# Kernel optimization log

Measured on AMD Instinct MI355X. Metric: run time of the kernel, lower is better.

Reference implementation:

```python
import jax, jax.numpy as jnp
import numpy as np

NUM_EXPERTS = 8
CAPACITY_C = 1.0
ROUTER_TEMP = 1.0
EPS = 1e-10


def reference(x, router_w, router_b, w_gate, b_gate, w_up, b_up, w_down, b_down):
    # x: [B, S, H]
    B, S, H = x.shape
    n_tok = B * S
    k = int(n_tok * CAPACITY_C) // NUM_EXPERTS  # expert capacity (1024 here)

    xf = x.reshape(n_tok, H)  # (b s) h

    # Linear router (dropout p=0 -> identity), computed in float32 as in .float()
    clean_h = xf @ router_w + router_b  # [n_tok, E]

    # Gumbel noise (deterministic key stands in for torch.rand_like)
    u = jax.random.uniform(jax.random.key(42), clean_h.shape, dtype=clean_h.dtype)
    gumbel = -jnp.log(-jnp.log(u + EPS) + EPS)
    h = (clean_h + gumbel) / ROUTER_TEMP

    Sm = jax.nn.softmax(h, axis=-1)  # softmax over experts

    # top-k over the TOKEN dim (dim=0) per expert -> expert-choice routing
    Gt, idxt = jax.lax.top_k(Sm.T, k)  # [E, k]
    G = Gt.T            # [k, E] routing weights
    idx = idxt.T        # [k, E] chosen token indices

    # Gather routed tokens (replaces the one-hot einsum gather exactly:
    # top-k indices are distinct per expert, so one-hot matmul == take)
    toks = jnp.take(xf, idx, axis=0)  # [k, E, H]

    # Shared SwiGLU FFN (group_size=1 -> one expert instance reused E times)
    gate = jax.nn.silu(toks @ w_gate + b_gate)  # [k, E, dff]
    up = toks @ w_up + b_up                      # [k, E, dff]
    e_out = (gate * up) @ w_down + b_down        # [k, E, H]

    # Weight by G and scatter-add back to token positions, summed over experts
    weighted = G[..., None] * e_out              # [k, E, H]
    y = jnp.zeros_like(xf).at[idx.reshape(-1)].add(weighted.reshape(-1, H))
    return y.reshape(B, S, H)


def setup_inputs() -> dict:
    key = jax.random.key(0)
    ks = jax.random.split(key, 6)
    B, S, H, E = 4, 2048, 2048, NUM_EXPERTS
    dff = int(H * 4 * 2 / 3)  # 5461
    sH = 1.0 / np.sqrt(H)
    sF = 1.0 / np.sqrt(dff)
    return {
        "x": jax.random.normal(ks[0], (B, S, H), dtype=jnp.float32),
        "router_w": jax.random.normal(ks[1], (H, E), dtype=jnp.float32) * sH,
        "router_b": jnp.zeros((E,), dtype=jnp.float32),
        "w_gate": jax.random.normal(ks[2], (H, dff), dtype=jnp.float32) * sH,
        "b_gate": jnp.zeros((dff,), dtype=jnp.float32),
        "w_up": jax.random.normal(ks[3], (H, dff), dtype=jnp.float32) * sH,
        "b_up": jnp.zeros((dff,), dtype=jnp.float32),
        "w_down": jax.random.normal(ks[4], (dff, H), dtype=jnp.float32) * sF,
        "b_down": jnp.zeros((H,), dtype=jnp.float32),
    }
```

## Files before the change

### kernel.cpp

```cpp
#include <hip/hip_runtime.h>
#include <cstdint>
#include <cstddef>

#define N_TOK  8192
#define HDIM   2048
#define NEXP   8
#define KCAP   1024
#define DFF    5461
#define DFF_PB 5504
#define DFF_PA 5472

typedef unsigned short u16;
typedef short bf16x8 __attribute__((ext_vector_type(8)));
typedef float f32x4  __attribute__((ext_vector_type(4)));

__device__ __forceinline__ u16 f2bf(float f) {
  uint32_t u = __float_as_uint(f);
  uint32_t r = (u + 0x7FFFu + ((u >> 16) & 1u)) >> 16;
  return (u16)r;
}

__device__ __forceinline__ uint32_t rotl32(uint32_t v, int d) {
  return (v << d) | (v >> (32 - d));
}

__device__ uint32_t threefry_bits(uint32_t idx) {
  const uint32_t ks0 = 0u, ks1 = 42u, ks2 = 0u ^ 42u ^ 0x1BD11BDAu;
  uint32_t x0 = 0u + ks0;
  uint32_t x1 = idx + ks1;
#define TFR(d) { x0 += x1; x1 = rotl32(x1, d); x1 ^= x0; }
  TFR(13) TFR(15) TFR(26) TFR(6)
  x0 += ks1; x1 += ks2 + 1u;
  TFR(17) TFR(29) TFR(16) TFR(24)
  x0 += ks2; x1 += ks0 + 2u;
  TFR(13) TFR(15) TFR(26) TFR(6)
  x0 += ks0; x1 += ks1 + 3u;
  TFR(17) TFR(29) TFR(16) TFR(24)
  x0 += ks1; x1 += ks2 + 4u;
  TFR(13) TFR(15) TFR(26) TFR(6)
  x0 += ks2; x1 += ks0 + 5u;
#undef TFR
  return x0 ^ x1;
}

__global__ __launch_bounds__(256) void router_kernel(const float* __restrict__ x,
    const float* __restrict__ rw, const float* __restrict__ rb,
    float* __restrict__ SmT)
{
  const int lane = threadIdx.x & 63;
  const int wid  = threadIdx.x >> 6;
  const int t = blockIdx.x * 4 + wid;
  const float* xr = x + (size_t)t * HDIM;
  float acc[8] = {0.f,0.f,0.f,0.f,0.f,0.f,0.f,0.f};
#pragma unroll
  for (int it = 0; it < HDIM / 64; ++it) {
    int h = lane + it * 64;
    float xv = xr[h];
    const float4* wp = (const float4*)(rw + h * 8);
    float4 w0 = wp[0], w1 = wp[1];
    acc[0] = fmaf(xv, w0.x, acc[0]);
    acc[1] = fmaf(xv, w0.y, acc[1]);
    acc[2] = fmaf(xv, w0.z, acc[2]);
    acc[3] = fmaf(xv, w0.w, acc[3]);
    acc[4] = fmaf(xv, w1.x, acc[4]);
    acc[5] = fmaf(xv, w1.y, acc[5]);
    acc[6] = fmaf(xv, w1.z, acc[6]);
    acc[7] = fmaf(xv, w1.w, acc[7]);
  }
#pragma unroll
  for (int m = 32; m >= 1; m >>= 1) {
#pragma unroll
    for (int e = 0; e < 8; ++e) acc[e] += __shfl_xor(acc[e], m, 64);
  }
  if (lane == 0) {
    float h[8];
#pragma unroll
    for (int e = 0; e < 8; ++e) {
      uint32_t bits = threefry_bits((uint32_t)(t * 8 + e));
      float u = __uint_as_float((bits >> 9) | 0x3f800000u) - 1.0f;
      u = fmaxf(u, 0.0f);
      float g = -logf(-logf(u + 1e-10f) + 1e-10f);
      h[e] = acc[e] + rb[e] + g;
    }
    float mx = h[0];
#pragma unroll
    for (int e = 1; e < 8; ++e) mx = fmaxf(mx, h[e]);
    float ex[8]; float s = 0.f;
#pragma unroll
    for (int e = 0; e < 8; ++e) { ex[e] = expf(h[e] - mx); s += ex[e]; }
#pragma unroll
    for (int e = 0; e < 8; ++e) SmT[e * N_TOK + t] = ex[e] / s;
  }
}

__global__ __launch_bounds__(1024) void select_topk(const float* __restrict__ SmT,
    uint32_t* __restrict__ selTok, float* __restrict__ selW)
{
  const int e = blockIdx.x;
  const int tid = threadIdx.x;
  const float* v = SmT + (size_t)e * N_TOK;
  __shared__ uint32_t hist[256];
  __shared__ uint32_t sh_byte, sh_kk, sh_cnt, sh_eqc;
  uint32_t bitsv[8];
#pragma unroll
  for (int i = 0; i < 8; ++i) bitsv[i] = __float_as_uint(v[tid + i * 1024]);
  uint32_t prefix = 0;
  uint32_t kk = KCAP;
  for (int s = 3; s >= 0; --s) {
    if (tid < 256) hist[tid] = 0;
    __syncthreads();
    uint32_t himask = (s == 3) ? 0u : (0xFFFFFFFFu << ((s + 1) * 8));
#pragma unroll
    for (int i = 0; i < 8; ++i) {
      uint32_t b = bitsv[i];
      if ((b & himask) == prefix) atomicAdd(&hist[(b >> (s * 8)) & 255u], 1u);
    }
    __syncthreads();
    if (tid == 0) {
      uint32_t cum = 0; uint32_t bsel = 0, kn = kk;
      for (int b = 255; b >= 0; --b) {
        uint32_t c = hist[b];
        if (cum + c >= kk) { bsel = (uint32_t)b; kn = kk - cum; break; }
        cum += c;
      }
      sh_byte = bsel; sh_kk = kn;
    }
    __syncthreads();
    prefix |= sh_byte << (s * 8);
    kk = sh_kk;
  }
  const uint32_t T = prefix;
  const uint32_t need = kk;
  if (tid == 0) { sh_cnt = 0; sh_eqc = 0; }
  __syncthreads();
#pragma unroll
  for (int i = 0; i < 8; ++i) {
    uint32_t b = bitsv[i];
    if (b > T) {
      uint32_t p = atomicAdd(&sh_cnt, 1u);
      selTok[e * KCAP + p] = (uint32_t)(tid + i * 1024);
      selW[e * KCAP + p] = __uint_as_float(b);
    } else if (b == T) {
      atomicAdd(&sh_eqc, 1u);
    }
  }
  __syncthreads();
  if (sh_eqc == need) {
#pragma unroll
    for (int i = 0; i < 8; ++i) {
      if (bitsv[i] == T) {
        uint32_t p = atomicAdd(&sh_cnt, 1u);
        selTok[e * KCAP + p] = (uint32_t)(tid + i * 1024);
        selW[e * KCAP + p] = __uint_as_float(T);
      }
    }
  } else if (tid == 0) {
    uint32_t p = sh_cnt, rem = need;
    for (int t = 0; t < N_TOK && rem > 0u; ++t) {
      if (__float_as_uint(v[t]) == T) {
        selTok[e * KCAP + p] = (uint32_t)t;
        selW[e * KCAP + p] = __uint_as_float(T);
        ++p; --rem;
      }
    }
  }
}

__global__ __launch_bounds__(256) void gather_kernel(const float* __restrict__ x,
    const uint32_t* __restrict__ selTok, u16* __restrict__ Xsel)
{
  const int slot = blockIdx.x;
  const int tid = threadIdx.x;
  const uint32_t tok = selTok[slot];
  const float4* src = (const float4*)(x + (size_t)tok * HDIM);
  float4 a = src[tid * 2], b = src[tid * 2 + 1];
  union { u16 h[8]; uint4 vv; } pk;
  pk.h[0] = f2bf(a.x); pk.h[1] = f2bf(a.y); pk.h[2] = f2bf(a.z); pk.h[3] = f2bf(a.w);
  pk.h[4] = f2bf(b.x); pk.h[5] = f2bf(b.y); pk.h[6] = f2bf(b.z); pk.h[7] = f2bf(b.w);
  ((uint4*)(Xsel + (size_t)slot * HDIM))[tid] = pk.vv;
}

__global__ __launch_bounds__(256) void pad_act_kernel(u16* __restrict__ act) {
  int idx = blockIdx.x * 256 + threadIdx.x;
  int row = idx / 11, col = idx % 11;
  act[(size_t)row * DFF_PA + (DFF + col)] = 0;
}

__global__ __launch_bounds__(256) void transpose_convert(const float* __restrict__ in,
    int rows_in, int cols_in, u16* __restrict__ out, int out_cols)
{
  __shared__ float tile[32][33];
  const int bi = blockIdx.y;
  const int bj = blockIdx.x;
  const int tx = threadIdx.x, ty = threadIdx.y;
#pragma unroll
  for (int t = 0; t < 4; ++t) {
    int r = bi * 32 + ty + t * 8, c = bj * 32 + tx;
    float vv = (r < rows_in && c < cols_in) ? in[(size_t)r * cols_in + c] : 0.0f;
    tile[ty + t * 8][tx] = vv;
  }
  __syncthreads();
#pragma unroll
  for (int t = 0; t < 4; ++t) {
    int oj = bj * 32 + ty + t * 8;
    int oi = bi * 32 + tx;
    out[(size_t)oj * out_cols + oi] = f2bf(tile[tx][ty + t * 8]);
  }
}

#if defined(__has_builtin)
#  if __has_builtin(__builtin_amdgcn_global_load_lds)
#    define HAVE_GLD 1
#  endif
#endif
#ifdef HAVE_GLD
#define GLD16(gp, lp) __builtin_amdgcn_global_load_lds( \
    (const __attribute__((address_space(1))) void*)(gp), \
    (__attribute__((address_space(3))) void*)(lp), 16, 0, 0)
#endif

__global__ __launch_bounds__(256, 2) void gemm1_kernel(
    const u16* __restrict__ Xsel,
    const u16* __restrict__ WgT,
    const u16* __restrict__ WuT,
    const float* __restrict__ bg, const float* __restrict__ bu,
    u16* __restrict__ act)
{
  const int id = blockIdx.x;
  const int sc = id >> 9;
  const int rem = id & 511;
  const int bm = rem & 63;
  const int bn = sc * 8 + (rem >> 6);
  if (bn >= 86) return;

  __shared__ u16 As [128 * 32];
  __shared__ u16 Bgs[ 64 * 32];
  __shared__ u16 Bus[ 64 * 32];
  const int tid = threadIdx.x;
  const int lane = tid & 63, wid = tid >> 6;
  const int wr = wid >> 1, wc = wid & 1;
  const int c0 = tid, c1 = tid + 256;
  const int r0 = c0 >> 2, ko0 = ((c0 & 3) ^ (r0 & 3)) * 8;
  const int r1 = c1 >> 2, ko1 = ((c1 & 3) ^ (r1 & 3)) * 8;
  const int rbq = tid >> 2, kob = ((tid & 3) ^ (rbq & 3)) * 8;

  const u16* a_g0  = Xsel + (size_t)(bm * 128 + r0) * HDIM + ko0;
  const u16* a_g1  = Xsel + (size_t)(bm * 128 + r1) * HDIM + ko1;
  const u16* bg_g  = WgT  + (size_t)(bn * 64 + rbq) * HDIM + kob;
  const u16* bu_g  = WuT  + (size_t)(bn * 64 + rbq) * HDIM + kob;
  u16* a_l0 = As  + c0 * 8; u16* a_l1 = As + c1 * 8;
  u16* g_l  = Bgs + tid * 8;
  u16* u_l  = Bus + tid * 8;

  f32x4 accg[4][2], accu[4][2];
  const f32x4 z4 = {0.f, 0.f, 0.f, 0.f};
#pragma unroll
  for (int i = 0; i < 4; ++i)
#pragma unroll
    for (int j = 0; j < 2; ++j) { accg[i][j] = z4; accu[i][j] = z4; }

  const int fr = lane & 15;
  const int ck = lane >> 4;
  const int sw = ck ^ (fr & 3);
  const int aoff = (wr * 64 + fr) * 32 + sw * 8;
  const int boff = (wc * 32 + fr) * 32 + sw * 8;

  for (int k0 = 0; k0 < HDIM; k0 += 32) {
#ifdef HAVE_GLD
    GLD16(a_g0 + k0, a_l0); GLD16(a_g1 + k0, a_l1);
    GLD16(bg_g + k0, g_l);  GLD16(bu_g + k0, u_l);
#else
    *(bf16x8*)a_l0 = *(const bf16x8*)(a_g0 + k0);
    *(bf16x8*)a_l1 = *(const bf16x8*)(a_g1 + k0);
    *(bf16x8*)g_l  = *(const bf16x8*)(bg_g + k0);
    *(bf16x8*)u_l  = *(const bf16x8*)(bu_g + k0);
#endif
    __syncthreads();
    bf16x8 af[4], bgf[2], buf2[2];
#pragma unroll
    for (int i = 0; i < 4; ++i) af[i] = *(const bf16x8*)&As[aoff + i * 16 * 32];
#pragma unroll
    for (int j = 0; j < 2; ++j) {
      bgf[j]  = *(const bf16x8*)&Bgs[boff + j * 16 * 32];
      buf2[j] = *(const bf16x8*)&Bus[boff + j * 16 * 32];
    }
#pragma unroll
    for (int i = 0; i < 4; ++i)
#pragma unroll
      for (int j = 0; j < 2; ++j) {
        accg[i][j] = __builtin_amdgcn_mfma_f32_16x16x32_bf16(af[i], bgf[j],  accg[i][j], 0, 0, 0);
        accu[i][j] = __builtin_amdgcn_mfma_f32_16x16x32_bf16(af[i], buf2[j], accu[i][j], 0, 0, 0);
      }
    __syncthreads();
  }
  const int rv = (lane >> 4) * 4;
#pragma unroll
  for (int i = 0; i < 4; ++i) {
#pragma unroll
    for (int v = 0; v < 4; ++v) {
      const int row = bm * 128 + wr * 64 + i * 16 + rv + v;
      u16* arow = act + (size_t)row * DFF_PA;
#pragma unroll
      for (int j = 0; j < 2; ++j) {
        const int col = bn * 64 + wc * 32 + j * 16 + fr;
        if (col < DFF) {
          float gv = accg[i][j][v] + bg[col];
          float uv = accu[i][j][v] + bu[col];
          float sv = gv / (1.0f + expf(-gv));
          arow[col] = f2bf(sv * uv);
        }
      }
    }
  }
}

__global__ __launch_bounds__(256, 2) void gemm2_kernel(
    const u16* __restrict__ act,
    const u16* __restrict__ WdT,
    const float* __restrict__ bd,
    const uint32_t* __restrict__ selTok,
    const float* __restrict__ selW,
    float* __restrict__ y)
{
  const int id = blockIdx.x;
  const int sc = id >> 9;
  const int rem = id & 511;
  const int bm = rem & 63;
  const int bn = sc * 8 + (rem >> 6);

  __shared__ u16 As[128 * 32];
  __shared__ u16 Bs[128 * 32];
  const int tid = threadIdx.x;
  const int lane = tid & 63, wid = tid >> 6;
  const int wr = wid >> 1, wc = wid & 1;
  const int c0 = tid, c1 = tid + 256;
  const int r0 = c0 >> 2, ko0 = ((c0 & 3) ^ (r0 & 3)) * 8;
  const int r1 = c1 >> 2, ko1 = ((c1 & 3) ^ (r1 & 3)) * 8;

  const u16* a_g0 = act + (size_t)(bm * 128 + r0) * DFF_PA + ko0;
  const u16* a_g1 = act + (size_t)(bm * 128 + r1) * DFF_PA + ko1;
  const u16* b_g0 = WdT + (size_t)(bn * 128 + r0) * DFF_PA + ko0;
  const u16* b_g1 = WdT + (size_t)(bn * 128 + r1) * DFF_PA + ko1;
  u16* a_l0 = As + c0 * 8; u16* a_l1 = As + c1 * 8;
  u16* b_l0 = Bs + c0 * 8; u16* b_l1 = Bs + c1 * 8;

  f32x4 acc[4][4];
  const f32x4 z4 = {0.f, 0.f, 0.f, 0.f};
#pragma unroll
  for (int i = 0; i < 4; ++i)
#pragma unroll
    for (int j = 0; j < 4; ++j) acc[i][j] = z4;

  const int fr = lane & 15;
  const int ck = lane >> 4;
  const int sw = ck ^ (fr & 3);
  const int aoff = (wr * 64 + fr) * 32 + sw * 8;
  const int boff = (wc * 64 + fr) * 32 + sw * 8;

  for (int k0 = 0; k0 < DFF_PA; k0 += 32) {
#ifdef HAVE_GLD
    GLD16(a_g0 + k0, a_l0); GLD16(a_g1 + k0, a_l1);
    GLD16(b_g0 + k0, b_l0); GLD16(b_g1 + k0, b_l1);
#else
    *(bf16x8*)a_l0 = *(const bf16x8*)(a_g0 + k0);
    *(bf16x8*)a_l1 = *(const bf16x8*)(a_g1 + k0);
    *(bf16x8*)b_l0 = *(const bf16x8*)(b_g0 + k0);
    *(bf16x8*)b_l1 = *(const bf16x8*)(b_g1 + k0);
#endif
    __syncthreads();
    bf16x8 af[4], bf[4];
#pragma unroll
    for (int i = 0; i < 4; ++i) af[i] = *(const bf16x8*)&As[aoff + i * 16 * 32];
#pragma unroll
    for (int j = 0; j < 4; ++j) bf[j] = *(const bf16x8*)&Bs[boff + j * 16 * 32];
#pragma unroll
    for (int i = 0; i < 4; ++i)
#pragma unroll
      for (int j = 0; j < 4; ++j)
        acc[i][j] = __builtin_amdgcn_mfma_f32_16x16x32_bf16(af[i], bf[j], acc[i][j], 0, 0, 0);
    __syncthreads();
  }
  const int rv = (lane >> 4) * 4;
#pragma unroll
  for (int i = 0; i < 4; ++i) {
#pragma unroll
    for (int v = 0; v < 4; ++v) {
      const int row = bm * 128 + wr * 64 + i * 16 + rv + v;
      const uint32_t tok = selTok[row];
      const float w = selW[row];
      float* yrow = y + (size_t)tok * HDIM;
#pragma unroll
      for (int j = 0; j < 4; ++j) {
        const int col = bn * 128 + wc * 64 + j * 16 + fr;
        atomicAdd(&yrow[col], w * (acc[i][j][v] + bd[col]));
      }
    }
  }
}

extern "C" void kernel_launch(void* const* d_in, const int* in_sizes, int n_in,
                              void* d_out, int out_size, void* d_ws, size_t ws_size,
                              hipStream_t stream) {
  const float* x      = (const float*)d_in[0];
  const float* rw     = (const float*)d_in[1];
  const float* rb     = (const float*)d_in[2];
  const float* w_gate = (const float*)d_in[3];
  const float* b_gate = (const float*)d_in[4];
  const float* w_up   = (const float*)d_in[5];
  const float* b_up   = (const float*)d_in[6];
  const float* w_down = (const float*)d_in[7];
  const float* b_down = (const float*)d_in[8];
  float* y = (float*)d_out;

  uint8_t* ws = (uint8_t*)d_ws;
  float*    SmT    = (float*)(ws + 0);
  uint32_t* selTok = (uint32_t*)(ws + 262144);
  float*    selW   = (float*)(ws + 294912);
  u16*      Xsel   = (u16*)(ws + 327680);
  u16*      WgT    = (u16*)(ws + 33882112ull);
  u16*      WuT    = (u16*)(ws + 56426496ull);
  u16*      WdT    = (u16*)(ws + 78970880ull);
  u16*      act    = (u16*)(ws + 101384192ull);

  hipMemsetAsync(d_out, 0, (size_t)N_TOK * HDIM * sizeof(float), stream);
  transpose_convert<<<dim3(172, 64), dim3(32, 8), 0, stream>>>(w_gate, 2048, DFF, WgT, 2048);
  transpose_convert<<<dim3(172, 64), dim3(32, 8), 0, stream>>>(w_up,   2048, DFF, WuT, 2048);
  transpose_convert<<<dim3(64, 171), dim3(32, 8), 0, stream>>>(w_down, DFF, 2048, WdT, DFF_PA);
  router_kernel<<<N_TOK / 4, 256, 0, stream>>>(x, rw, rb, SmT);
  select_topk<<<NEXP, 1024, 0, stream>>>(SmT, selTok, selW);
  gather_kernel<<<N_TOK, 256, 0, stream>>>(x, selTok, Xsel);
  pad_act_kernel<<<(N_TOK * 11) / 256, 256, 0, stream>>>(act);
  gemm1_kernel<<<11 * 512, 256, 0, stream>>>(Xsel, WgT, WuT, b_gate, b_up, act);
  gemm2_kernel<<<2 * 512, 256, 0, stream>>>(act, WdT, b_down, selTok, selW, y);
}
```

Baseline: 1.032 ms.

## Rework expert GEMMs into 256-row tiles with a 4-stage LDS pipeline

Both expert GEMMs move to 512-thread blocks with 256x128 and 256x256 output tiles and a four-buffer shared-memory ring. Global-to-LDS loads for three stages are kept in flight using explicit vmcnt waits and raw barriers. Each K step is split into two MFMA halves, with loads interleaved between them and wave priority raised around the MFMA work. Blocks are remapped across XCDs, and zeroing of the act padding moves into the gemm1 epilogue, so the separate pad kernel is dropped. The cost is about 128KB of LDS per block, which limits occupancy to one block per CU, and a fragile hand-written wait-count scheme.

```diff
diff --git a/kernel.cpp b/kernel.cpp
--- a/kernel.cpp
+++ b/kernel.cpp
@@ -180,12 +180,6 @@
   ((uint4*)(Xsel + (size_t)slot * HDIM))[tid] = pk.vv;
 }
 
-__global__ __launch_bounds__(256) void pad_act_kernel(u16* __restrict__ act) {
-  int idx = blockIdx.x * 256 + threadIdx.x;
-  int row = idx / 11, col = idx % 11;
-  act[(size_t)row * DFF_PA + (DFF + col)] = 0;
-}
-
 __global__ __launch_bounds__(256) void transpose_convert(const float* __restrict__ in,
     int rows_in, int cols_in, u16* __restrict__ out, int out_cols)
 {
@@ -217,104 +211,141 @@
 #define GLD16(gp, lp) __builtin_amdgcn_global_load_lds( \
     (const __attribute__((address_space(1))) void*)(gp), \
     (__attribute__((address_space(3))) void*)(lp), 16, 0, 0)
+#define STG(gp, lp) GLD16(gp, lp)
+#define WAIT_STAGE8() asm volatile("s_waitcnt vmcnt(8)" ::: "memory")
+#define WAIT_STAGE4() asm volatile("s_waitcnt vmcnt(4)" ::: "memory")
+#define WAIT_STAGE0() asm volatile("s_waitcnt vmcnt(0)" ::: "memory")
+#else
+#define STG(gp, lp) (*(bf16x8*)(lp) = *(const bf16x8*)(gp))
+#define WAIT_STAGE8() asm volatile("s_waitcnt vmcnt(0) lgkmcnt(0)" ::: "memory")
+#define WAIT_STAGE4() asm volatile("s_waitcnt vmcnt(0) lgkmcnt(0)" ::: "memory")
+#define WAIT_STAGE0() asm volatile("s_waitcnt vmcnt(0) lgkmcnt(0)" ::: "memory")
 #endif
-
-__global__ __launch_bounds__(256, 2) void gemm1_kernel(
+#define BARRIER() asm volatile("s_barrier" ::: "memory")
+
+__global__ __launch_bounds__(512, 2) void gemm1_kernel(
     const u16* __restrict__ Xsel,
     const u16* __restrict__ WgT,
     const u16* __restrict__ WuT,
     const float* __restrict__ bg, const float* __restrict__ bu,
     u16* __restrict__ act)
 {
+  __shared__ u16 As [4][256 * 32];
+  __shared__ u16 Bgs[4][128 * 32];
+  __shared__ u16 Bus[4][128 * 32];
+
   const int id = blockIdx.x;
-  const int sc = id >> 9;
-  const int rem = id & 511;
-  const int bm = rem & 63;
-  const int bn = sc * 8 + (rem >> 6);
-  if (bn >= 86) return;
-
-  __shared__ u16 As [128 * 32];
-  __shared__ u16 Bgs[ 64 * 32];
-  __shared__ u16 Bus[ 64 * 32];
+  const int wg = (id & 7) * 172 + (id >> 3);
+  const int bm = wg & 31;
+  const int bn = wg >> 5;
+
   const int tid = threadIdx.x;
+  const int c0 = tid, c1 = tid + 512;
+  const int r0 = c0 >> 2, p0 = ((c0 & 3) ^ ((r0 >> 1) & 3)) * 8;
+  const int r1 = c1 >> 2, p1 = ((c1 & 3) ^ ((r1 >> 1) & 3)) * 8;
+  const int rb = tid >> 2, pb = ((tid & 3) ^ ((rb >> 1) & 3)) * 8;
+  const u16* ag0 = Xsel + (size_t)(bm * 256 + r0) * HDIM + p0;
+  const u16* ag1 = Xsel + (size_t)(bm * 256 + r1) * HDIM + p1;
+  const u16* gg  = WgT  + (size_t)(bn * 128 + rb) * HDIM + pb;
+  const u16* ug  = WuT  + (size_t)(bn * 128 + rb) * HDIM + pb;
+
+#define G1_STAGE_A(tt) { u16* s_ = As[(tt) & 3]; \
+    STG(ag0 + (tt) * 32, s_ + c0 * 8); \
+    STG(ag1 + (tt) * 32, s_ + c1 * 8); }
+#define G1_STAGE_B(tt) { \
+    STG(gg + (tt) * 32, Bgs[(tt) & 3] + tid * 8); \
+    STG(ug + (tt) * 32, Bus[(tt) & 3] + tid * 8); }
+
+  f32x4 accg[8][2], accu[8][2];
+  const f32x4 z4 = {0.f, 0.f, 0.f, 0.f};
+#pragma unroll
+  for (int i = 0; i < 8; ++i)
+#pragma unroll
+    for (int j = 0; j < 2; ++j) { accg[i][j] = z4; accu[i][j] = z4; }
+
   const int lane = tid & 63, wid = tid >> 6;
-  const int wr = wid >> 1, wc = wid & 1;
-  const int c0 = tid, c1 = tid + 256;
-  const int r0 = c0 >> 2, ko0 = ((c0 & 3) ^ (r0 & 3)) * 8;
-  const int r1 = c1 >> 2, ko1 = ((c1 & 3) ^ (r1 & 3)) * 8;
-  const int rbq = tid >> 2, kob = ((tid & 3) ^ (rbq & 3)) * 8;
-
-  const u16* a_g0  = Xsel + (size_t)(bm * 128 + r0) * HDIM + ko0;
-  const u16* a_g1  = Xsel + (size_t)(bm * 128 + r1) * HDIM + ko1;
-  const u16* bg_g  = WgT  + (size_t)(bn * 64 + rbq) * HDIM + kob;
-  const u16* bu_g  = WuT  + (size_t)(bn * 64 + rbq) * HDIM + kob;
-  u16* a_l0 = As  + c0 * 8; u16* a_l1 = As + c1 * 8;
-  u16* g_l  = Bgs + tid * 8;
-  u16* u_l  = Bus + tid * 8;
-
-  f32x4 accg[4][2], accu[4][2];
-  const f32x4 z4 = {0.f, 0.f, 0.f, 0.f};
-#pragma unroll
-  for (int i = 0; i < 4; ++i)
-#pragma unroll
-    for (int j = 0; j < 2; ++j) { accg[i][j] = z4; accu[i][j] = z4; }
-
-  const int fr = lane & 15;
-  const int ck = lane >> 4;
-  const int sw = ck ^ (fr & 3);
-  const int aoff = (wr * 64 + fr) * 32 + sw * 8;
-  const int boff = (wc * 32 + fr) * 32 + sw * 8;
-
-  for (int k0 = 0; k0 < HDIM; k0 += 32) {
-#ifdef HAVE_GLD
-    GLD16(a_g0 + k0, a_l0); GLD16(a_g1 + k0, a_l1);
-    GLD16(bg_g + k0, g_l);  GLD16(bu_g + k0, u_l);
-#else
-    *(bf16x8*)a_l0 = *(const bf16x8*)(a_g0 + k0);
-    *(bf16x8*)a_l1 = *(const bf16x8*)(a_g1 + k0);
-    *(bf16x8*)g_l  = *(const bf16x8*)(bg_g + k0);
-    *(bf16x8*)u_l  = *(const bf16x8*)(bu_g + k0);
-#endif
-    __syncthreads();
-    bf16x8 af[4], bgf[2], buf2[2];
-#pragma unroll
-    for (int i = 0; i < 4; ++i) af[i] = *(const bf16x8*)&As[aoff + i * 16 * 32];
+  const int wm = wid >> 2, wn = wid & 3;
+  const int fr = lane & 15, ck = lane >> 4;
+  const int sw8 = (ck ^ ((fr >> 1) & 3)) * 8;
+  const int aoff = (wm * 128 + fr) * 32 + sw8;
+  const int boff = (wn * 32 + fr) * 32 + sw8;
+
+  G1_STAGE_A(0) G1_STAGE_B(0)
+  G1_STAGE_A(1) G1_STAGE_B(1)
+  G1_STAGE_A(2) G1_STAGE_B(2)
+  WAIT_STAGE8(); BARRIER();
+
+  for (int t = 0; t < 64; ++t) {
+    const u16* Ab = As[t & 3];
+    const u16* Gb = Bgs[t & 3];
+    const u16* Ub = Bus[t & 3];
+    bf16x8 a0[4], gf[2], uf[2];
+#pragma unroll
+    for (int i = 0; i < 4; ++i) a0[i] = *(const bf16x8*)&Ab[aoff + i * (16 * 32)];
 #pragma unroll
     for (int j = 0; j < 2; ++j) {
-      bgf[j]  = *(const bf16x8*)&Bgs[boff + j * 16 * 32];
-      buf2[j] = *(const bf16x8*)&Bus[boff + j * 16 * 32];
-    }
+      gf[j] = *(const bf16x8*)&Gb[boff + j * (16 * 32)];
+      uf[j] = *(const bf16x8*)&Ub[boff + j * (16 * 32)];
+    }
+    if (t + 3 < 64) G1_STAGE_A(t + 3)
+    BARRIER();
+    __builtin_amdgcn_s_setprio(1);
 #pragma unroll
     for (int i = 0; i < 4; ++i)
 #pragma unroll
       for (int j = 0; j < 2; ++j) {
-        accg[i][j] = __builtin_amdgcn_mfma_f32_16x16x32_bf16(af[i], bgf[j],  accg[i][j], 0, 0, 0);
-        accu[i][j] = __builtin_amdgcn_mfma_f32_16x16x32_bf16(af[i], buf2[j], accu[i][j], 0, 0, 0);
-      }
-    __syncthreads();
-  }
-  const int rv = (lane >> 4) * 4;
-#pragma unroll
-  for (int i = 0; i < 4; ++i) {
+        accg[i][j] = __builtin_amdgcn_mfma_f32_16x16x32_bf16(a0[i], gf[j], accg[i][j], 0, 0, 0);
+        accu[i][j] = __builtin_amdgcn_mfma_f32_16x16x32_bf16(a0[i], uf[j], accu[i][j], 0, 0, 0);
+      }
+    __builtin_amdgcn_s_setprio(0);
+    BARRIER();
+    bf16x8 a1[4];
+#pragma unroll
+    for (int i = 0; i < 4; ++i) a1[i] = *(const bf16x8*)&Ab[aoff + (64 + i * 16) * 32];
+    if (t + 3 < 64) G1_STAGE_B(t + 3)
+    BARRIER();
+    __builtin_amdgcn_s_setprio(1);
+#pragma unroll
+    for (int i = 0; i < 4; ++i)
+#pragma unroll
+      for (int j = 0; j < 2; ++j) {
+        accg[4 + i][j] = __builtin_amdgcn_mfma_f32_16x16x32_bf16(a1[i], gf[j], accg[4 + i][j], 0, 0, 0);
+        accu[4 + i][j] = __builtin_amdgcn_mfma_f32_16x16x32_bf16(a1[i], uf[j], accu[4 + i][j], 0, 0, 0);
+      }
+    __builtin_amdgcn_s_setprio(0);
+    if (t < 61)      { WAIT_STAGE8(); }
+    else if (t == 61){ WAIT_STAGE4(); }
+    else             { WAIT_STAGE0(); }
+    BARRIER();
+  }
+
+  const int rv = ck * 4;
+#pragma unroll
+  for (int i8 = 0; i8 < 8; ++i8) {
 #pragma unroll
     for (int v = 0; v < 4; ++v) {
-      const int row = bm * 128 + wr * 64 + i * 16 + rv + v;
+      const int row = bm * 256 + wm * 128 + i8 * 16 + rv + v;
       u16* arow = act + (size_t)row * DFF_PA;
 #pragma unroll
       for (int j = 0; j < 2; ++j) {
-        const int col = bn * 64 + wc * 32 + j * 16 + fr;
-        if (col < DFF) {
-          float gv = accg[i][j][v] + bg[col];
-          float uv = accu[i][j][v] + bu[col];
-          float sv = gv / (1.0f + expf(-gv));
-          arow[col] = f2bf(sv * uv);
+        const int col = bn * 128 + wn * 32 + j * 16 + fr;
+        if (col < DFF_PA) {
+          u16 ov = 0;
+          if (col < DFF) {
+            float gv = accg[i8][j][v] + bg[col];
+            float uv = accu[i8][j][v] + bu[col];
+            ov = f2bf((gv / (1.0f + expf(-gv))) * uv);
+          }
+          arow[col] = ov;
         }
       }
     }
   }
-}
-
-__global__ __launch_bounds__(256, 2) void gemm2_kernel(
+#undef G1_STAGE_A
+#undef G1_STAGE_B
+}
+
+__global__ __launch_bounds__(512, 2) void gemm2_kernel(
     const u16* __restrict__ act,
     const u16* __restrict__ WdT,
     const float* __restrict__ bd,
@@ -322,80 +353,104 @@
     const float* __restrict__ selW,
     float* __restrict__ y)
 {
+  __shared__ u16 As[4][256 * 32];
+  __shared__ u16 Bs[4][256 * 32];
+
   const int id = blockIdx.x;
-  const int sc = id >> 9;
-  const int rem = id & 511;
-  const int bm = rem & 63;
-  const int bn = sc * 8 + (rem >> 6);
-
-  __shared__ u16 As[128 * 32];
-  __shared__ u16 Bs[128 * 32];
+  const int wg = (id & 7) * 32 + (id >> 3);
+  const int bm = wg & 31;
+  const int bn = wg >> 5;
+
   const int tid = threadIdx.x;
+  const int c0 = tid, c1 = tid + 512;
+  const int r0 = c0 >> 2, p0 = ((c0 & 3) ^ ((r0 >> 1) & 3)) * 8;
+  const int r1 = c1 >> 2, p1 = ((c1 & 3) ^ ((r1 >> 1) & 3)) * 8;
+  const u16* ag0 = act + (size_t)(bm * 256 + r0) * DFF_PA + p0;
+  const u16* ag1 = act + (size_t)(bm * 256 + r1) * DFF_PA + p1;
+  const u16* bg0 = WdT + (size_t)(bn * 256 + r0) * DFF_PA + p0;
+  const u16* bg1 = WdT + (size_t)(bn * 256 + r1) * DFF_PA + p1;
+
+#define G2_STAGE_A(tt) { u16* s_ = As[(tt) & 3]; \
+    STG(ag0 + (tt) * 32, s_ + c0 * 8); \
+    STG(ag1 + (tt) * 32, s_ + c1 * 8); }
+#define G2_STAGE_B(tt) { u16* s_ = Bs[(tt) & 3]; \
+    STG(bg0 + (tt) * 32, s_ + c0 * 8); \
+    STG(bg1 + (tt) * 32, s_ + c1 * 8); }
+
+  f32x4 acc[8][4];
+  const f32x4 z4 = {0.f, 0.f, 0.f, 0.f};
+#pragma unroll
+  for (int i = 0; i < 8; ++i)
+#pragma unroll
+    for (int j = 0; j < 4; ++j) acc[i][j] = z4;
+
   const int lane = tid & 63, wid = tid >> 6;
-  const int wr = wid >> 1, wc = wid & 1;
-  const int c0 = tid, c1 = tid + 256;
-  const int r0 = c0 >> 2, ko0 = ((c0 & 3) ^ (r0 & 3)) * 8;
-  const int r1 = c1 >> 2, ko1 = ((c1 & 3) ^ (r1 & 3)) * 8;
-
-  const u16* a_g0 = act + (size_t)(bm * 128 + r0) * DFF_PA + ko0;
-  const u16* a_g1 = act + (size_t)(bm * 128 + r1) * DFF_PA + ko1;
-  const u16* b_g0 = WdT + (size_t)(bn * 128 + r0) * DFF_PA + ko0;
-  const u16* b_g1 = WdT + (size_t)(bn * 128 + r1) * DFF_PA + ko1;
-  u16* a_l0 = As + c0 * 8; u16* a_l1 = As + c1 * 8;
-  u16* b_l0 = Bs + c0 * 8; u16* b_l1 = Bs + c1 * 8;
-
-  f32x4 acc[4][4];
-  const f32x4 z4 = {0.f, 0.f, 0.f, 0.f};
-#pragma unroll
-  for (int i = 0; i < 4; ++i)
-#pragma unroll
-    for (int j = 0; j < 4; ++j) acc[i][j] = z4;
-
-  const int fr = lane & 15;
-  const int ck = lane >> 4;
-  const int sw = ck ^ (fr & 3);
-  const int aoff = (wr * 64 + fr) * 32 + sw * 8;
-  const int boff = (wc * 64 + fr) * 32 + sw * 8;
-
-  for (int k0 = 0; k0 < DFF_PA; k0 += 32) {
-#ifdef HAVE_GLD
-    GLD16(a_g0 + k0, a_l0); GLD16(a_g1 + k0, a_l1);
-    GLD16(b_g0 + k0, b_l0); GLD16(b_g1 + k0, b_l1);
-#else
-    *(bf16x8*)a_l0 = *(const bf16x8*)(a_g0 + k0);
-    *(bf16x8*)a_l1 = *(const bf16x8*)(a_g1 + k0);
-    *(bf16x8*)b_l0 = *(const bf16x8*)(b_g0 + k0);
-    *(bf16x8*)b_l1 = *(const bf16x8*)(b_g1 + k0);
-#endif
-    __syncthreads();
-    bf16x8 af[4], bf[4];
-#pragma unroll
-    for (int i = 0; i < 4; ++i) af[i] = *(const bf16x8*)&As[aoff + i * 16 * 32];
-#pragma unroll
-    for (int j = 0; j < 4; ++j) bf[j] = *(const bf16x8*)&Bs[boff + j * 16 * 32];
+  const int wm = wid >> 2, wn = wid & 3;
+  const int fr = lane & 15, ck = lane >> 4;
+  const int sw8 = (ck ^ ((fr >> 1) & 3)) * 8;
+  const int aoff = (wm * 128 + fr) * 32 + sw8;
+  const int boff = (wn * 64 + fr) * 32 + sw8;
+
+  G2_STAGE_A(0) G2_STAGE_B(0)
+  G2_STAGE_A(1) G2_STAGE_B(1)
+  G2_STAGE_A(2) G2_STAGE_B(2)
+  WAIT_STAGE8(); BARRIER();
+
+  const int NT = DFF_PA / 32;
+  for (int t = 0; t < NT; ++t) {
+    const u16* Ab = As[t & 3];
+    const u16* Bb = Bs[t & 3];
+    bf16x8 a0[4], bf[4];
+#pragma unroll
+    for (int i = 0; i < 4; ++i) a0[i] = *(const bf16x8*)&Ab[aoff + i * (16 * 32)];
+#pragma unroll
+    for (int j = 0; j < 4; ++j) bf[j] = *(const bf16x8*)&Bb[boff + j * (16 * 32)];
+    if (t + 3 < NT) G2_STAGE_A(t + 3)
+    BARRIER();
+    __builtin_amdgcn_s_setprio(1);
 #pragma unroll
     for (int i = 0; i < 4; ++i)
 #pragma unroll
       for (int j = 0; j < 4; ++j)
-        acc[i][j] = __builtin_amdgcn_mfma_f32_16x16x32_bf16(af[i], bf[j], acc[i][j], 0, 0, 0);
-    __syncthreads();
-  }
-  const int rv = (lane >> 4) * 4;
-#pragma unroll
-  for (int i = 0; i < 4; ++i) {
+        acc[i][j] = __builtin_amdgcn_mfma_f32_16x16x32_bf16(a0[i], bf[j], acc[i][j], 0, 0, 0);
+    __builtin_amdgcn_s_setprio(0);
+    BARRIER();
+    bf16x8 a1[4];
+#pragma unroll
+    for (int i = 0; i < 4; ++i) a1[i] = *(const bf16x8*)&Ab[aoff + (64 + i * 16) * 32];
+    if (t + 3 < NT) G2_STAGE_B(t + 3)
+    BARRIER();
+    __builtin_amdgcn_s_setprio(1);
+#pragma unroll
+    for (int i = 0; i < 4; ++i)
+#pragma unroll
+      for (int j = 0; j < 4; ++j)
+        acc[4 + i][j] = __builtin_amdgcn_mfma_f32_16x16x32_bf16(a1[i], bf[j], acc[4 + i][j], 0, 0, 0);
+    __builtin_amdgcn_s_setprio(0);
+    if (t < NT - 3)       { WAIT_STAGE8(); }
+    else if (t == NT - 3) { WAIT_STAGE4(); }
+    else                  { WAIT_STAGE0(); }
+    BARRIER();
+  }
+
+  const int rv = ck * 4;
+#pragma unroll
+  for (int i8 = 0; i8 < 8; ++i8) {
 #pragma unroll
     for (int v = 0; v < 4; ++v) {
-      const int row = bm * 128 + wr * 64 + i * 16 + rv + v;
-      const uint32_t tok = selTok[row];
-      const float w = selW[row];
+      const int srow = bm * 256 + wm * 128 + i8 * 16 + rv + v;
+      const uint32_t tok = selTok[srow];
+      const float w = selW[srow];
       float* yrow = y + (size_t)tok * HDIM;
 #pragma unroll
       for (int j = 0; j < 4; ++j) {
-        const int col = bn * 128 + wc * 64 + j * 16 + fr;
-        atomicAdd(&yrow[col], w * (acc[i][j][v] + bd[col]));
-      }
-    }
-  }
+        const int col = bn * 256 + wn * 64 + j * 16 + fr;
+        atomicAdd(&yrow[col], w * (acc[i8][j][v] + bd[col]));
+      }
+    }
+  }
+#undef G2_STAGE_A
+#undef G2_STAGE_B
 }
 
 extern "C" void kernel_launch(void* const* d_in, const int* in_sizes, int n_in,
@@ -429,7 +484,6 @@
   router_kernel<<<N_TOK / 4, 256, 0, stream>>>(x, rw, rb, SmT);
   select_topk<<<NEXP, 1024, 0, stream>>>(SmT, selTok, selW);
   gather_kernel<<<N_TOK, 256, 0, stream>>>(x, selTok, Xsel);
-  pad_act_kernel<<<(N_TOK * 11) / 256, 256, 0, stream>>>(act);
-  gemm1_kernel<<<11 * 512, 256, 0, stream>>>(Xsel, WgT, WuT, b_gate, b_up, act);
-  gemm2_kernel<<<2 * 512, 256, 0, stream>>>(act, WdT, b_down, selTok, selW, y);
-}
+  gemm1_kernel<<<43 * 32, 512, 0, stream>>>(Xsel, WgT, WuT, b_gate, b_up, act);
+  gemm2_kernel<<<8 * 32, 512, 0, stream>>>(act, WdT, b_down, selTok, selW, y);
+}
```

After: 1.089 ms. +5.6%, slower.
